# Kernel tuning notes

Measured on AMD Instinct MI355X. Metric: run time of the kernel, lower is better.

The kernel has to match this reference:

```python
import jax, jax.numpy as jnp
import numpy as np

B, S, V, E, HL = 64, 30, 5000, 300, 256
TWOH = 2 * HL
KB, MAPD, MEMD, MLP, NCLS = 512, 512, 512, 1024, 32
L, T, NMOD, NOPS = 8, 9, 9, 6
IH, IW, CIN = 15, 10, 512 + 128


def setup_inputs():
    key = jax.random.key(0)
    ks = iter(jax.random.split(key, 64))
    g = lambda shape, s=0.05: jax.random.normal(next(ks), shape, jnp.float32) * s
    inp = {}
    inp['image'] = g((B, CIN, IH, IW), 1.0)
    inp['ques'] = jax.random.randint(next(ks), (B, S), 0, V)
    ql = jnp.sort(jax.random.randint(next(ks), (B,), 1, S + 1))[::-1]
    inp['q_len'] = ql.at[0].set(S)
    inp['embed_W'] = g((V, E))
    for d in ('f', 'b'):
        inp['lstm_Wi_' + d] = g((E, 4 * HL))
        inp['lstm_Wh_' + d] = g((HL, 4 * HL))
        inp['lstm_b_' + d] = jnp.zeros((4 * HL,), jnp.float32)
    inp['W1'] = g((T, TWOH, TWOH))
    inp['b_1'] = jnp.zeros((TWOH,), jnp.float32)
    inp['W2_w'] = g((2 * TWOH, TWOH)); inp['W2_b'] = jnp.zeros((TWOH,), jnp.float32)
    inp['W3'] = g((TWOH,))
    inp['c_0'] = g((TWOH,), 1.0)
    inp['Wmod'] = g((TWOH, NMOD))
    inp['ic1_w'] = g((KB, CIN)); inp['ic1_b'] = g((KB,), 1.0)
    inp['ic2_w'] = g((KB, KB)); inp['ic2_b'] = g((KB,), 1.0)
    inp['i2m_w'] = g((MAPD, KB)); inp['i2m_b'] = g((MAPD,), 1.0)
    inp['t2m_w'] = g((TWOH, MAPD)); inp['t2m_b'] = jnp.zeros((MAPD,), jnp.float32)
    inp['cell3_ow'] = g((4, NOPS), 1.0)
    inp['cell3_cw'] = g((4, MAPD)); inp['cell3_cb'] = jnp.zeros((4,), jnp.float32)
    inp['cell4_ow'] = g((2, NOPS), 1.0)
    inp['cell4_cw'] = g((2, MAPD)); inp['cell4_cb'] = jnp.zeros((2,), jnp.float32)
    inp['ans_ow'] = g((2, NOPS), 1.0)
    inp['ans_W'] = g((2, 2 * MAPD, MEMD)); inp['ans_b'] = jnp.zeros((2, MEMD), jnp.float32)
    inp['out1_w'] = g((TWOH + MEMD, MLP)); inp['out1_b'] = jnp.zeros((MLP,), jnp.float32)
    inp['out2_w'] = g((MLP, NCLS)); inp['out2_b'] = jnp.zeros((NCLS,), jnp.float32)
    return inp


def _conv1x1(x, w, b):
    return jnp.einsum('bchw,oc->bohw', x, w) + b[None, :, None, None]


def _lstm_dir(xW, Wh, mask, reverse):
    # xW: [S,B,4H], mask: [S,B,1] ; torch LSTM gate order i,f,g,o
    Bn, Hn = xW.shape[1], Wh.shape[0]
    def step(carry, inp):
        h, c = carry
        xw, m = inp
        z = xw + h @ Wh
        i, f, gg, o = jnp.split(z, 4, axis=-1)
        cn = jax.nn.sigmoid(f) * c + jax.nn.sigmoid(i) * jnp.tanh(gg)
        hn = jax.nn.sigmoid(o) * jnp.tanh(cn)
        return (jnp.where(m, hn, h), jnp.where(m, cn, c)), jnp.where(m, hn, 0.0)
    init = (jnp.zeros((Bn, Hn), xW.dtype), jnp.zeros((Bn, Hn), xW.dtype))
    (hF, _), outs = jax.lax.scan(step, init, (xW, mask), reverse=reverse)
    return hF, outs


def _mix3(ow, x, a, t):
    # soft op mixing (DARTS-style) for 3-input cells: x [B,D,H,W], a [B,H,W], t [B,D]
    w = jax.nn.softmax(ow)
    a4 = a[:, None]; t4 = t[:, :, None, None]
    ops = (x * t4, x + t4, x * a4, x * t4 * a4, x, a4 * t4)
    return jax.nn.elu(sum(w[k] * ops[k] for k in range(NOPS)))


def _mix4(ow, x, a1, a2, t):
    w = jax.nn.softmax(ow)
    a14 = a1[:, None]; a24 = a2[:, None]; t4 = t[:, :, None, None]
    ops = (x * t4, x + t4, x * a14, x * a24, x * a14 * a24, x * t4 * (a14 + a24))
    return jax.nn.elu(sum(w[k] * ops[k] for k in range(NOPS)))


def _forward(image, ques, q_len, embed_W, lstm_Wi_f, lstm_Wh_f, lstm_b_f, lstm_Wi_b, lstm_Wh_b, lstm_b_b, W1, b_1, W2_w, W2_b, W3, c_0, Wmod, ic1_w, ic1_b, ic2_w, ic2_b, i2m_w, i2m_b, t2m_w, t2m_b, cell3_ow, cell3_cw, cell3_cb, cell4_ow, cell4_cw, cell4_cb, ans_ow, ans_W, ans_b, out1_w, out1_b, out2_w, out2_b):
    # img_conv (1x1 conv -> ELU -> 1x1 conv)
    x = jax.nn.elu(_conv1x1(image, ic1_w, ic1_b))
    x = _conv1x1(x, ic2_w, ic2_b)
    Bn, _, Hh, Ww = x.shape
    Sn = ques.shape[1]
    # bi-LSTM over the (packed, i.e. masked) question
    emb = embed_W[ques]                                   # [B,S,E]
    mask = (jnp.arange(Sn)[None, :] < q_len[:, None])     # [B,S]
    mT = mask.T[:, :, None].astype(x.dtype) > 0           # [S,B,1] bool
    xWf = (emb @ lstm_Wi_f + lstm_b_f).transpose(1, 0, 2)
    xWb = (emb @ lstm_Wi_b + lstm_b_b).transpose(1, 0, 2)
    hF, oF = _lstm_dir(xWf, lstm_Wh_f, mT, False)
    hB, oB = _lstm_dir(xWb, lstm_Wh_b, mT, True)
    lstm_out = jnp.concatenate([oF, oB], -1).transpose(1, 0, 2)  # [B,S,2H], zero at pads
    q = jnp.concatenate([hF, hB], -1)                            # [B,2H]
    img_map = _conv1x1(x, i2m_w, i2m_b)                          # [B,MAP,H,W]
    stack = jnp.zeros((Bn, Hh, Ww, L), x.dtype)
    p = jnp.zeros((Bn, L), x.dtype).at[:, 0].set(1.0)
    mem = jnp.zeros((Bn, MEMD), x.dtype)
    c_prev = jnp.tile(c_0[None], (Bn, 1))
    e0 = jnp.zeros((L,), x.dtype).at[0].set(1.0)
    imp_loss = jnp.float32(0.0)
    read = lambda st, pp: jnp.einsum('bhwl,bl->bhw', st, pp)
    dec = lambda pp: jnp.concatenate([pp[:, 1:], jnp.zeros_like(pp[:, :1])], 1) + pp * e0
    for t in range(T):
        u = jnp.concatenate([q @ W1[t] + b_1, c_prev], 1) @ W2_w + W2_b  # [B,2H]
        wl = u @ Wmod                                                     # [B,9]
        ls = jax.nn.log_softmax(wl, axis=1)
        imp_loss = imp_loss - jnp.sum(jnp.exp(ls) * ls)
        w = jnp.exp(ls)
        attn = jax.nn.softmax(jnp.einsum('bsh,h->bs', lstm_out * u[:, None, :], W3), axis=1)
        c = jnp.einsum('bs,bsh->bh', attn, lstm_out)
        c_prev = c
        tmap = c @ t2m_w + t2m_b
        stacks, ps = [], []
        a_top = read(stack, p)     # attention at stack top
        # modules 0-3: overwrite at current pointer (pointer shift is commented out in source)
        for m in range(4):
            out = jnp.einsum('bdhw,d->bhw', _mix3(cell3_ow[m], img_map, a_top, tmap), cell3_cw[m]) + cell3_cb[m]
            pb = p[:, None, None, :]
            stacks.append(stack * (1.0 - pb) + out[..., None] * pb)
            ps.append(p)
        # modules 4-5: pop one (soft pointer decrement), then write
        p_dec = dec(p)
        a2 = read(stack, p_dec)
        for m in range(2):
            out = jnp.einsum('bdhw,d->bhw', _mix4(cell4_ow[m], img_map, a_top, a2, tmap), cell4_cw[m]) + cell4_cb[m]
            pb = p_dec[:, None, None, :]
            stacks.append(stack * (1.0 - pb) + out[..., None] * pb)
            ps.append(p_dec)
        # modules 6-7: answer cells -> memory update, stack untouched
        pooled6 = jnp.mean(_mix3(ans_ow[0], img_map, a_top, tmap), axis=(2, 3))
        mem6 = jnp.concatenate([pooled6, tmap], 1) @ ans_W[0] + ans_b[0]
        stacks.append(stack); ps.append(p)
        pooled7 = jnp.mean(_mix4(ans_ow[1], img_map, a_top, a2, tmap), axis=(2, 3))
        mem7 = jnp.concatenate([pooled7, tmap], 1) @ ans_W[1] + ans_b[1]
        stacks.append(stack); ps.append(p_dec)
        # module 8: NoOp
        stacks.append(stack); ps.append(p)
        # soft mixing over modules (the scatter-heavy part)
        stack = jnp.einsum('bm,bmhwl->bhwl', w, jnp.stack(stacks, 1))
        p = jnp.einsum('bm,bml->bl', w, jnp.stack(ps, 1))
        mem = w[:, 6:7] * mem6 + w[:, 7:8] * mem7 + (1.0 - w[:, 6:7] - w[:, 7:8]) * mem
    h1 = jax.nn.elu(jnp.concatenate([q, mem], 1) @ out1_w + out1_b)
    logits = h1 @ out2_w + out2_b
    return logits, imp_loss


def reference(image, ques, q_len, embed_W, lstm_Wi_f, lstm_Wh_f, lstm_b_f, lstm_Wi_b, lstm_Wh_b, lstm_b_b, W1, b_1, W2_w, W2_b, W3, c_0, Wmod, ic1_w, ic1_b, ic2_w, ic2_b, i2m_w, i2m_b, t2m_w, t2m_b, cell3_ow, cell3_cw, cell3_cb, cell4_ow, cell4_cw, cell4_cb, ans_ow, ans_W, ans_b, out1_w, out1_b, out2_w, out2_b):
    return _forward(image, ques, q_len, embed_W, lstm_Wi_f, lstm_Wh_f, lstm_b_f, lstm_Wi_b, lstm_Wh_b, lstm_b_b, W1, b_1, W2_w, W2_b, W3, c_0, Wmod, ic1_w, ic1_b, ic2_w, ic2_b, i2m_w, i2m_b, t2m_w, t2m_b, cell3_ow, cell3_cw, cell3_cb, cell4_ow, cell4_cw, cell4_cb, ans_ow, ans_W, ans_b, out1_w, out1_b, out2_w, out2_b)
```

## Files before the change

kernel.cpp:

```cpp
#include <hip/hip_runtime.h>
#include <hip/hip_fp16.h>
#include <math.h>

#define DEV __device__ __forceinline__

DEV float fexp(float x){ return __expf(x); }
DEV float elu_(float x){ return x > 0.f ? x : fexp(x) - 1.f; }
DEV float sigm_(float x){ return 1.f/(1.f + fexp(-x)); }
DEV float tanh_(float x){ float e = fexp(2.f*x); return 1.f - 2.f/(e + 1.f); }
DEV unsigned bf16r(float x){ unsigned u = __float_as_uint(x);
  return (u + 0x7fffu + ((u>>16)&1u)) >> 16; }
DEV float blo(unsigned u){ return __uint_as_float(u << 16); }
DEV float bhi(unsigned u){ return __uint_as_float(u & 0xffff0000u); }
DEV float bl(unsigned short u){ return __uint_as_float(((unsigned)u) << 16); }

using frag  = __attribute__((ext_vector_type(8))) short;
using fragh = __attribute__((ext_vector_type(8))) _Float16;
using f32x4 = __attribute__((ext_vector_type(4))) float;

DEV uint4 cload16w(const void* p){
  uint4 r;
  asm volatile("global_load_dwordx4 %0, %1, off sc0 sc1\n\ts_waitcnt vmcnt(0)"
               : "=v"(r) : "v"(p) : "memory");
  return r;
}
DEV uint4 cload16nw(const void* p){
  uint4 r;
  asm volatile("global_load_dwordx4 %0, %1, off sc0 sc1"
               : "=v"(r) : "v"(p) : "memory");
  return r;
}

DEV void d_packB(const float* __restrict__ W, short* __restrict__ Bp,
                 int KC, int Ng, int Ksrc, int N, int trans, int idx)
{
  if (idx >= KC*Ng*64) return;
  int lane = idx & 63;
  int g    = (idx >> 6) % Ng;
  int kc   = idx / (64*Ng);
  int n = g*16 + (lane & 15);
  int kb = kc*32 + ((lane >> 4) << 3);
  unsigned o[4];
#pragma unroll
  for (int jj = 0; jj < 4; ++jj) {
    int k0 = kb + 2*jj;
    float v0 = (k0   < Ksrc) ? (trans ? W[(size_t)n*Ksrc + k0]   : W[(size_t)(k0)*N + n])   : 0.f;
    float v1 = (k0+1 < Ksrc) ? (trans ? W[(size_t)n*Ksrc + k0+1] : W[(size_t)(k0+1)*N + n]) : 0.f;
    o[jj] = bf16r(v0) | (bf16r(v1) << 16);
  }
  *(uint4*)(Bp + (size_t)idx*8) = make_uint4(o[0], o[1], o[2], o[3]);
}

DEV void d_packImg(const float* __restrict__ image, short* __restrict__ Ap, int idx)
{
  int lane = idx & 63;
  int kc   = (idx >> 6) % 20;
  int mt   = idx / 1280;
  int row = mt*16 + (lane & 15);
  int b = row / 150, p = row % 150;
  int cb = kc*32 + ((lane >> 4) << 3);
  unsigned o[4];
#pragma unroll
  for (int jj = 0; jj < 4; ++jj) {
    float v0 = image[((size_t)b*640 + cb + 2*jj    )*150 + p];
    float v1 = image[((size_t)b*640 + cb + 2*jj + 1)*150 + p];
    o[jj] = bf16r(v0) | (bf16r(v1) << 16);
  }
  *(uint4*)(Ap + (size_t)idx*8) = make_uint4(o[0], o[1], o[2], o[3]);
}

DEV void d_packEmb(const float* __restrict__ embedW, const int* __restrict__ ques,
                   short* __restrict__ Ap, int idx)
{
  int lane = idx & 63;
  int kc   = (idx >> 6) % 10;
  int mt   = idx / 640;
  int row = mt*16 + (lane & 15);
  int q = ques[row];
  int kb = kc*32 + ((lane >> 4) << 3);
  unsigned o[4];
#pragma unroll
  for (int jj = 0; jj < 4; ++jj) {
    int k0 = kb + 2*jj;
    float v0 = (k0   < 300) ? embedW[(size_t)q*300 + k0]   : 0.f;
    float v1 = (k0+1 < 300) ? embedW[(size_t)q*300 + k0+1] : 0.f;
    o[jj] = bf16r(v0) | (bf16r(v1) << 16);
  }
  *(uint4*)(Ap + (size_t)idx*8) = make_uint4(o[0], o[1], o[2], o[3]);
}

__global__ __launch_bounds__(256)
void megapack_k(const float* __restrict__ c0, const float* __restrict__ c3ow,
                const float* __restrict__ c4ow, const float* __restrict__ aow,
                float* __restrict__ stack, float* __restrict__ pvecA,
                float* __restrict__ mem, float* __restrict__ cprev,
                float* __restrict__ swb, float* __restrict__ pl,
                const float* __restrict__ Whf, const float* __restrict__ Whb,
                unsigned* __restrict__ whT,
                float* __restrict__ hbufz, int* __restrict__ flagz,
                const float* __restrict__ ic1w, short* __restrict__ w1p,
                const float* __restrict__ ic2w, short* __restrict__ w2mp,
                const float* __restrict__ i2mw, short* __restrict__ w3mp,
                const float* __restrict__ Wif, short* __restrict__ wifp,
                const float* __restrict__ Wib, short* __restrict__ wibp,
                const float* __restrict__ image, short* __restrict__ imgP,
                const float* __restrict__ embedW, const int* __restrict__ ques,
                short* __restrict__ embp,
                const float* __restrict__ t2mw, unsigned* __restrict__ t2pp,
                const float* __restrict__ W2w, unsigned short* __restrict__ w2bp,
                const float* __restrict__ ansW, unsigned short* __restrict__ answp)
{
  const int bx = blockIdx.x, tid = threadIdx.x;
  if (bx < 320) {
    int idx = bx*256 + tid;
    int stride = 320*256;
    for (int i = idx; i < 64*150*8; i += stride) stack[i] = 0.f;
    for (int i = idx; i < 64*8;    i += stride) pvecA[i] = ((i & 7) == 0) ? 1.f : 0.f;
    for (int i = idx; i < 64*512;  i += stride) mem[i] = 0.f;
    for (int i = idx; i < 64*512;  i += stride) cprev[i] = c0[i & 511];
    for (int i = idx; i < 9*2*64*512; i += stride) pl[i] = 0.f;
    for (int i = idx; i < 32768;   i += stride) hbufz[i] = 0.f;
    if (idx < 256) flagz[idx] = 0;
    if (idx < 8) {
      const float* ow = (idx < 4) ? (c3ow + idx*6)
                      : (idx < 6) ? (c4ow + (idx-4)*6)
                                  : (aow  + (idx-6)*6);
      float mx = ow[0];
      for (int m = 1; m < 6; ++m) mx = fmaxf(mx, ow[m]);
      float e[6]; float s = 0.f;
      for (int m = 0; m < 6; ++m) { e[m] = fexp(ow[m]-mx); s += e[m]; }
      for (int m = 0; m < 6; ++m) swb[idx*6+m] = e[m]/s;
    }
  } else if (bx < 1344) {
    int idx = (bx-320)*256 + tid;
    int dd  = idx >> 17;
    int rem = idx & 131071;
    int kp  = rem >> 10;
    int zc  = rem & 1023;
    const float* Wh = dd ? Whb : Whf;
    __half2 hv = __floats2half2_rn(Wh[(size_t)(2*kp)*1024 + zc],
                                   Wh[(size_t)(2*kp+1)*1024 + zc]);
    whT[((size_t)dd << 17) + (zc << 7) + kp] = *(unsigned*)&hv;
  } else if (bx < 1504) {
    d_packB(ic1w, w1p, 20, 32, 640, 512, 1, (bx-1344)*256 + tid);
  } else if (bx < 1632) {
    d_packB(ic2w, w2mp, 16, 32, 512, 512, 1, (bx-1504)*256 + tid);
  } else if (bx < 1760) {
    d_packB(i2mw, w3mp, 16, 32, 512, 512, 1, (bx-1632)*256 + tid);
  } else if (bx < 1920) {
    d_packB(Wif, wifp, 10, 64, 300, 1024, 0, (bx-1760)*256 + tid);
  } else if (bx < 2080) {
    d_packB(Wib, wibp, 10, 64, 300, 1024, 0, (bx-1920)*256 + tid);
  } else if (bx < 5080) {
    d_packImg(image, imgP, (bx-2080)*256 + tid);
  } else if (bx < 5380) {
    d_packEmb(embedW, ques, embp, (bx-5080)*256 + tid);
  } else if (bx < 5892) {
    int idx = (bx-5380)*256 + tid;
    int k = idx >> 8, c = idx & 255;
    t2pp[idx] = bf16r(t2mw[(size_t)k*512 + c]) | (bf16r(t2mw[(size_t)k*512 + 256 + c]) << 16);
  } else if (bx < 7940) {
    int i = (bx-5892)*256 + tid;
    w2bp[i] = (unsigned short)bf16r(W2w[i]);
  } else {
    int i = (bx-7940)*256 + tid;
    answp[i] = (unsigned short)bf16r(ansW[i]);
  }
}

__global__ __launch_bounds__(256)
void gemmM_k(const short* __restrict__ ApA, const short* __restrict__ ApB,
             const short* __restrict__ BpA, const short* __restrict__ BpB,
             const float* __restrict__ biasA, const float* __restrict__ biasB,
             void* __restrict__ CoutA, void* __restrict__ CoutB,
             int KC, int Ng, int N, int mode, int act, int KCout)
{
  __shared__ float lds[4][16][68];
  const int z = blockIdx.z;
  const short* Ap = z ? ApB : ApA;
  const short* Bp = z ? BpB : BpA;
  const float* bias = z ? biasB : biasA;
  void* Cout = z ? CoutB : CoutA;
  const int tid = threadIdx.x, lane = tid & 63, w = tid >> 6;
  const int mt = blockIdx.y*4 + w;
  const int ncol0 = blockIdx.x*64;
  const short* Abase = Ap + (((size_t)mt*KC) << 9) + lane*8;
  const short* Bbase = Bp + (((size_t)blockIdx.x*4) << 9) + lane*8;
  f32x4 acc0 = {0.f,0.f,0.f,0.f}, acc1 = acc0, acc2 = acc0, acc3 = acc0;
#pragma unroll 2
  for (int kc = 0; kc < KC; ++kc) {
    frag a = *(const frag*)(Abase + ((size_t)kc << 9));
    const short* bk = Bbase + (((size_t)kc*Ng) << 9);
    frag b0 = *(const frag*)(bk);
    frag b1 = *(const frag*)(bk + 512);
    frag b2 = *(const frag*)(bk + 1024);
    frag b3 = *(const frag*)(bk + 1536);
    acc0 = __builtin_amdgcn_mfma_f32_16x16x32_bf16(a, b0, acc0, 0, 0, 0);
    acc1 = __builtin_amdgcn_mfma_f32_16x16x32_bf16(a, b1, acc1, 0, 0, 0);
    acc2 = __builtin_amdgcn_mfma_f32_16x16x32_bf16(a, b2, acc2, 0, 0, 0);
    acc3 = __builtin_amdgcn_mfma_f32_16x16x32_bf16(a, b3, acc3, 0, 0, 0);
  }
  {
    int colb = lane & 15, rowb = (lane >> 4)*4;
#pragma unroll
    for (int r = 0; r < 4; ++r) {
      lds[w][rowb+r][ 0+colb] = acc0[r];
      lds[w][rowb+r][16+colb] = acc1[r];
      lds[w][rowb+r][32+colb] = acc2[r];
      lds[w][rowb+r][48+colb] = acc3[r];
    }
  }
  __syncthreads();
  if (mode == 0) {
    float* C = (float*)Cout;
    int mloc = lane >> 2, q4 = lane & 3;
    size_t rowoff = (size_t)(mt*16 + mloc)*N + ncol0 + q4*16;
#pragma unroll
    for (int i = 0; i < 4; ++i) {
      float4 v = *(float4*)&lds[w][mloc][q4*16 + i*4];
      const float* bp = bias + ncol0 + q4*16 + i*4;
      v.x += bp[0]; v.y += bp[1]; v.z += bp[2]; v.w += bp[3];
      if (act) { v.x = elu_(v.x); v.y = elu_(v.y); v.z = elu_(v.z); v.w = elu_(v.w); }
      *(float4*)&C[rowoff + i*4] = v;
    }
  } else if (mode == 1) {
    short* C = (short*)Cout;
    int m = lane & 15, qb = (lane >> 4)*8;
#pragma unroll
    for (int h = 0; h < 2; ++h) {
      int nl = h*32 + qb;
      unsigned o[4];
#pragma unroll
      for (int jj = 0; jj < 4; ++jj) {
        float v0 = lds[w][m][nl + 2*jj]     + bias[ncol0 + nl + 2*jj];
        float v1 = lds[w][m][nl + 2*jj + 1] + bias[ncol0 + nl + 2*jj + 1];
        if (act) { v0 = elu_(v0); v1 = elu_(v1); }
        o[jj] = bf16r(v0) | (bf16r(v1) << 16);
      }
      *(uint4*)(C + (((size_t)mt*KCout + (ncol0 >> 5) + h) << 9) + lane*8)
          = make_uint4(o[0], o[1], o[2], o[3]);
    }
  } else {
    unsigned short* C = (unsigned short*)Cout;
    int row = lane >> 2, cb = (lane & 3)*16;
#pragma unroll
    for (int h = 0; h < 2; ++h) {
      unsigned o[4];
#pragma unroll
      for (int jj = 0; jj < 4; ++jj) {
        float v0 = lds[w][row][cb + h*8 + 2*jj]     + bias[ncol0 + cb + h*8 + 2*jj];
        float v1 = lds[w][row][cb + h*8 + 2*jj + 1] + bias[ncol0 + cb + h*8 + 2*jj + 1];
        if (act) { v0 = elu_(v0); v1 = elu_(v1); }
        o[jj] = bf16r(v0) | (bf16r(v1) << 16);
      }
      *(uint4*)&C[(size_t)(mt*16 + row)*N + ncol0 + cb + h*8]
          = make_uint4(o[0], o[1], o[2], o[3]);
    }
  }
}

__global__ __launch_bounds__(512)
void gemm64b_k(const float* __restrict__ A1, long zA1, int K1log,
               const float* __restrict__ A2, int K2,
               const float* __restrict__ B, long zB,
               const float* __restrict__ bias, int zbias,
               float* __restrict__ C, long zC, int N, int act)
{
  const int K1 = 1 << K1log;
  const int Kt = K1 + K2;
  __shared__ __align__(16) float As[8][1024];
  __shared__ float part[8][8][64];
  const int tid = threadIdx.x;
  const int z = blockIdx.z;
  const int r0 = blockIdx.y*8;
  {
    const float* a1 = A1 + (size_t)z*zA1;
    const int nf4 = (8*K1) >> 2;
    for (int e4 = tid; e4 < nf4; e4 += 512) {
      int r = e4 >> (K1log-2);
      int k4 = (e4 & ((K1>>2)-1)) << 2;
      *(float4*)&As[r][k4] = *(const float4*)&a1[(size_t)(r0+r)*K1 + k4];
    }
    if (K2 > 0) {
      for (int e4 = tid; e4 < 1024; e4 += 512) {
        int r = e4 >> 7;
        int k4 = (e4 & 127) << 2;
        *(float4*)&As[r][K1+k4] = *(const float4*)&A2[(size_t)(r0+r)*512 + k4];
      }
    }
  }
  __syncthreads();
  const int lane = tid & 63, w = tid >> 6;
  const int n = blockIdx.x*64 + lane;
  const bool nv = n < N;
  const int kseg = Kt >> 3;
  const int k0 = w*kseg;
  const float* Bp = B + (size_t)z*zB + (size_t)k0*N + (nv ? n : 0);
  float acc[8] = {0,0,0,0,0,0,0,0};
#pragma unroll 8
  for (int kk = 0; kk < kseg; ++kk) {
    float bv = nv ? Bp[(size_t)kk*N] : 0.f;
    int k = k0 + kk;
#pragma unroll
    for (int r = 0; r < 8; ++r) acc[r] += As[r][k]*bv;
  }
#pragma unroll
  for (int r = 0; r < 8; ++r) part[w][r][lane] = acc[r];
  __syncthreads();
  {
    int r = tid >> 6, c = tid & 63;
    int nn = blockIdx.x*64 + c;
    if (nn < N) {
      float s = 0.f;
#pragma unroll
      for (int w2 = 0; w2 < 8; ++w2) s += part[w2][r][c];
      s += bias ? bias[(size_t)z*zbias + nn] : 0.f;
      if (act == 1) s = elu_(s);
      C[(size_t)z*zC + (size_t)(r0+r)*N + nn] = s;
    }
  }
}

__global__ __launch_bounds__(256)
void lstmM_k(const float* __restrict__ xWf, const float* __restrict__ xWb,
             const unsigned* __restrict__ whT, const int* __restrict__ qlen,
             unsigned long long* __restrict__ hbuf, int* __restrict__ flags,
             float* __restrict__ lstm_out, float* __restrict__ qout)
{
  const int bx = blockIdx.x;
  const int d = bx & 1, g = (bx >> 1) & 3, n = bx >> 3;
  const int tid = threadIdx.x, lane = tid & 63, w = tid >> 6;
  const int q = lane >> 4, cl = lane & 15;
  __shared__ __align__(16) unsigned short Wl[65536];

#pragma unroll 4
  for (int rb = 0; rb < 32; ++rb) {
    int lcrow = rb*8 + (tid >> 5);
    int gt = lcrow >> 6, c = lcrow & 63;
    int zc = gt*256 + n*64 + c;
    uint4 v = *(const uint4*)(whT + (((size_t)d*1024 + zc) << 7) + ((tid & 31) << 2));
    int byteoff = (lcrow << 9) + ((((tid & 31) << 4)) ^ ((lcrow & 7) << 4));
    *(uint4*)((char*)Wl + byteoff) = v;
  }

  const float* xW = d ? xWb : xWf;
  const int b   = g*16 + cl;
  const int c4  = w*16 + q*4;
  const int hc4 = n*64 + c4;
  const int len = qlen[b];
  float cst[4] = {0.f,0.f,0.f,0.f}, hst[4] = {0.f,0.f,0.f,0.f};
  int* flg = flags + ((d*4 + g) << 2);
  const int bofs = (cl & 7) << 4;
  __syncthreads();

  for (int ss = 0; ss < 30; ++ss) {
    const int s = d ? (29 - ss) : ss;
    const float* xr = xW + (size_t)b*30720 + (size_t)s*1024 + hc4;
    f32x4 xwv[4];
#pragma unroll
    for (int gt = 0; gt < 4; ++gt) xwv[gt] = *(const f32x4*)(xr + gt*256);

    if (ss > 0) {
      for (;;) {
        uint4 f4 = cload16w(flg);
        if ((int)f4.x >= ss && (int)f4.y >= ss &&
            (int)f4.z >= ss && (int)f4.w >= ss) break;
      }
      __builtin_amdgcn_sched_barrier(0);
    }
    const char* hbr = (const char*)(hbuf + ((size_t)(((ss & 1)*2 + d)*4 + g) << 9))
                    + (cl << 9) + (q << 4);
    union { uint4 u; fragh f; } hv[8];
#pragma unroll
    for (int ks = 0; ks < 8; ++ks) hv[ks].u = cload16nw(hbr + (ks << 6));
    asm volatile("s_waitcnt vmcnt(0)" ::: "memory");
    __builtin_amdgcn_sched_barrier(0);

    f32x4 acc0 = {0.f,0.f,0.f,0.f}, acc1 = acc0, acc2 = acc0, acc3 = acc0;
#pragma unroll
    for (int ks = 0; ks < 8; ++ks) {
      const int kb = ((ks << 6) + (q << 4)) ^ bofs;
      const char* wb = (const char*)Wl + ((w*16 + cl) << 9) + kb;
      fragh a0 = *(const fragh*)(wb);
      fragh a1 = *(const fragh*)(wb + (64 << 9));
      fragh a2 = *(const fragh*)(wb + (128 << 9));
      fragh a3 = *(const fragh*)(wb + (192 << 9));
      acc0 = __builtin_amdgcn_mfma_f32_16x16x32_f16(a0, hv[ks].f, acc0, 0, 0, 0);
      acc1 = __builtin_amdgcn_mfma_f32_16x16x32_f16(a1, hv[ks].f, acc1, 0, 0, 0);
      acc2 = __builtin_amdgcn_mfma_f32_16x16x32_f16(a2, hv[ks].f, acc2, 0, 0, 0);
      acc3 = __builtin_amdgcn_mfma_f32_16x16x32_f16(a3, hv[ks].f, acc3, 0, 0, 0);
    }
    const bool m = s < len;
    f32x4 lo4;
    float hvv[4];
#pragma unroll
    for (int r = 0; r < 4; ++r) {
      float iv = acc0[r] + xwv[0][r];
      float fv = acc1[r] + xwv[1][r];
      float gv = acc2[r] + xwv[2][r];
      float o_ = acc3[r] + xwv[3][r];
      float cn = sigm_(fv)*cst[r] + sigm_(iv)*tanh_(gv);
      float hn = sigm_(o_)*tanh_(cn);
      float hk = m ? hn : hst[r];
      cst[r] = m ? cn : cst[r];
      hst[r] = hk;
      hvv[r] = hk;
      lo4[r] = m ? hn : 0.f;
    }
    unsigned long long* hbw = hbuf + ((size_t)((((ss & 1) ^ 1)*2 + d)*4 + g) << 9);
    union { unsigned long long u; __half2 h2[2]; } hp;
    hp.h2[0] = __floats2half2_rn(hvv[0], hvv[1]);
    hp.h2[1] = __floats2half2_rn(hvv[2], hvv[3]);
    __hip_atomic_store(hbw + cl*64 + (hc4 >> 2), hp.u,
                       __ATOMIC_RELAXED, __HIP_MEMORY_SCOPE_AGENT);
    *(f32x4*)(lstm_out + (((size_t)b*30 + s) << 9) + (d << 8) + hc4) = lo4;
    asm volatile("s_waitcnt vmcnt(0)" ::: "memory");
    __syncthreads();
    if (tid == 0)
      __hip_atomic_store(&flg[n], ss + 1, __ATOMIC_RELAXED, __HIP_MEMORY_SCOPE_AGENT);
  }
  *(f32x4*)(qout + ((size_t)b << 9) + (d << 8) + hc4) =
      f32x4{hst[0], hst[1], hst[2], hst[3]};
}

__global__ __launch_bounds__(1024)
void kcattn3_k(const float* __restrict__ u, const float* __restrict__ Wmod,
               const float* __restrict__ lstm_out, const float* __restrict__ W3,
               const unsigned* __restrict__ t2pp, const float* __restrict__ t2mb,
               float* __restrict__ woutAll, float* __restrict__ imp_part,
               float* __restrict__ cout, float* __restrict__ tmapv, int t)
{
  int b = blockIdx.x;
  int tid = threadIdx.x;
  int lane = tid & 63, wave = tid >> 6;
  __shared__ float ush[512];
  __shared__ float sC[512];
  __shared__ float cpart[512];
  __shared__ float tpart[4][512];
  __shared__ float wl[9];
  __shared__ float sc[32], at[32];
  if (tid < 512) ush[tid] = u[b*512 + tid];
  __syncthreads();
  for (int s = wave; s < 30; s += 16) {
    float acc = 0.f;
    const float* lo = lstm_out + ((size_t)b*30 + s)*512;
#pragma unroll
    for (int h = lane; h < 512; h += 64) acc += lo[h]*ush[h]*W3[h];
#pragma unroll
    for (int off = 32; off; off >>= 1) acc += __shfl_down(acc, off);
    if (lane == 0) sc[s] = acc;
  }
  if (wave < 9) {
    float acc = 0.f;
#pragma unroll
    for (int k = lane; k < 512; k += 64) acc += ush[k]*Wmod[k*9+wave];
#pragma unroll
    for (int off = 32; off; off >>= 1) acc += __shfl_down(acc, off);
    if (lane == 0) wl[wave] = acc;
  }
  __syncthreads();
  if (tid == 0) {
    float mx = wl[0];
    for (int m = 1; m < 9; ++m) mx = fmaxf(mx, wl[m]);
    float s = 0.f;
    for (int m = 0; m < 9; ++m) s += fexp(wl[m]-mx);
    float ls = logf(s);
    float ent = 0.f;
    for (int m = 0; m < 9; ++m) {
      float l = wl[m]-mx-ls;
      float w = fexp(l);
      woutAll[t*576 + b*9 + m] = w;
      ent -= w*l;
    }
    imp_part[t*64+b] = ent;
  }
  if (wave == 1) {
    float v = (lane < 30) ? sc[lane] : -3.4e38f;
    float mx = v;
#pragma unroll
    for (int off = 32; off; off >>= 1) mx = fmaxf(mx, __shfl_xor(mx, off));
    float e = (lane < 30) ? fexp(v-mx) : 0.f;
    float ssum = e;
#pragma unroll
    for (int off = 32; off; off >>= 1) ssum += __shfl_xor(ssum, off);
    if (lane < 30) at[lane] = e/ssum;
  }
  __syncthreads();
  {
    int h = tid & 511, seg = tid >> 9;
    float acc = 0.f;
    int s0 = seg ? 15 : 0, s1 = seg ? 30 : 15;
    for (int s = s0; s < s1; ++s) acc += at[s]*lstm_out[((size_t)b*30 + s)*512 + h];
    if (seg) cpart[h] = acc;
    __syncthreads();
    if (!seg) {
      float tot = acc + cpart[h];
      cout[b*512+h] = tot;
      sC[h] = tot;
    }
  }
  __syncthreads();
  {
    int c2 = tid & 255, ks = tid >> 8;
    float a0 = 0.f, a1 = 0.f;
    const unsigned* tp = t2pp + c2;
#pragma unroll 8
    for (int k = ks*128; k < ks*128 + 128; ++k) {
      float cv = sC[k];
      unsigned wv2 = tp[(size_t)k*256];
      a0 += cv*blo(wv2);
      a1 += cv*bhi(wv2);
    }
    tpart[ks][c2]       = a0;
    tpart[ks][256 + c2] = a1;
  }
  __syncthreads();
  if (tid < 512) {
    float v = tpart[0][tid] + tpart[1][tid] + tpart[2][tid] + tpart[3][tid];
    tmapv[b*512 + tid] = v + t2mb[tid];
  }
}

__global__ __launch_bounds__(256)
void modules2_k(const unsigned short* __restrict__ imapB, const float* __restrict__ tmapv,
                float* __restrict__ stack, const float* __restrict__ pvecIn,
                float* __restrict__ pvecOut,
                const float* __restrict__ swb, const float* __restrict__ c3w,
                const float* __restrict__ c3b, const float* __restrict__ c4w,
                const float* __restrict__ c4b, const float* __restrict__ wmod,
                float* __restrict__ plt)
{
  int b  = blockIdx.x;
  int pb = blockIdx.y;
  int lane = threadIdx.x & 63, wave = threadIdx.x >> 6;
  __shared__ float sT[512];
  __shared__ float pv[8], pd[8], wm[9];
  __shared__ float wpart[4][2][512];
  for (int j = threadIdx.x; j < 512; j += 256) sT[j] = tmapv[b*512 + j];
  if (threadIdx.x < 8) pv[threadIdx.x] = pvecIn[b*8+threadIdx.x];
  if (threadIdx.x >= 64 && threadIdx.x < 73) wm[threadIdx.x-64] = wmod[b*9 + threadIdx.x-64];
  __syncthreads();
  if (threadIdx.x < 8) {
    int l = threadIdx.x;
    pd[l] = (l < 7 ? pv[l+1] : 0.f) + (l == 0 ? pv[0] : 0.f);
  }
  __syncthreads();
  if (pb == 0 && threadIdx.x < 8) {
    int l = threadIdx.x;
    float WP = wm[0]+wm[1]+wm[2]+wm[3] + wm[6] + wm[8];
    float WD = wm[4]+wm[5] + wm[7];
    pvecOut[b*8+l] = WP*pv[l] + WD*pd[l];
  }

  float W[8][6];
#pragma unroll
  for (int m = 0; m < 8; ++m)
#pragma unroll
    for (int i = 0; i < 6; ++i) W[m][i] = swb[m*6+i];
  float W03 = wm[0]+wm[1]+wm[2]+wm[3];
  float W45 = wm[4]+wm[5];

  float acc6[8], acc7[8];
#pragma unroll
  for (int i = 0; i < 8; ++i) { acc6[i] = 0.f; acc7[i] = 0.f; }

  for (int pi = 0; pi < 2; ++pi) {
    int p = pb*8 + wave*2 + pi;
    if (p < 150) {
      const float* st = stack + ((size_t)b*150 + p)*8;
      float a = 0.f, av2 = 0.f;
#pragma unroll
      for (int l = 0; l < 8; ++l) { float v = st[l]; a += v*pv[l]; av2 += v*pd[l]; }
      float part[6] = {0,0,0,0,0,0};
#pragma unroll 2
      for (int i = 0; i < 8; ++i) {
        int d = i*64 + lane;
        float x = bl(imapB[((size_t)b*150 + p)*512 + d]);
        float t = sT[d];
#pragma unroll
        for (int m = 0; m < 4; ++m) {
          float c1 = W[m][0]*t + W[m][1] + W[m][4] + (W[m][2] + W[m][3]*t)*a;
          float c0 = W[m][1]*t + W[m][5]*t*a;
          part[m] += elu_(c1*x + c0) * c3w[m*512+d];
        }
#pragma unroll
        for (int m = 0; m < 2; ++m) {
          float c1 = W[4+m][0]*t + W[4+m][1] + W[4+m][2]*a + W[4+m][3]*av2
                   + W[4+m][4]*a*av2 + W[4+m][5]*t*(a+av2);
          part[4+m] += elu_(c1*x + W[4+m][1]*t) * c4w[m*512+d];
        }
        float c16 = W[6][0]*t + W[6][1] + W[6][4] + (W[6][2] + W[6][3]*t)*a;
        float c06 = W[6][1]*t + W[6][5]*t*a;
        acc6[i] += elu_(c16*x + c06);
        float c17 = W[7][0]*t + W[7][1] + W[7][2]*a + W[7][3]*av2
                  + W[7][4]*a*av2 + W[7][5]*t*(a+av2);
        acc7[i] += elu_(c17*x + W[7][1]*t);
      }
#pragma unroll
      for (int m = 0; m < 6; ++m) {
#pragma unroll
        for (int off = 32; off; off >>= 1) part[m] += __shfl_down(part[m], off);
        part[m] = __shfl(part[m], 0);
      }
      float r3  = wm[0]*(part[0]+c3b[0]) + wm[1]*(part[1]+c3b[1])
                + wm[2]*(part[2]+c3b[2]) + wm[3]*(part[3]+c3b[3]);
      float r45 = wm[4]*(part[4]+c4b[0]) + wm[5]*(part[5]+c4b[1]);
      if (lane < 8) {
        int l = lane;
        size_t idx = ((size_t)b*150 + p)*8 + l;
        stack[idx] = stack[idx]*(1.f - W03*pv[l] - W45*pd[l])
                   + pv[l]*r3 + pd[l]*r45;
      }
    }
  }
#pragma unroll
  for (int i = 0; i < 8; ++i) {
    wpart[wave][0][i*64+lane] = acc6[i];
    wpart[wave][1][i*64+lane] = acc7[i];
  }
  __syncthreads();
  for (int e = threadIdx.x; e < 1024; e += 256) {
    int which = e >> 9, d = e & 511;
    float s = wpart[0][which][d] + wpart[1][which][d]
            + wpart[2][which][d] + wpart[3][which][d];
    atomicAdd(&plt[(size_t)which*32768 + b*512 + d], s * (1.f/150.f));
  }
}

__global__ __launch_bounds__(512)
void ansu3_k(const float* __restrict__ plt, const float* __restrict__ tmapv,
             const unsigned short* __restrict__ answp, const float* __restrict__ ansb,
             float* __restrict__ m67o,
             const float* __restrict__ tmp1n, const float* __restrict__ cprev,
             const unsigned short* __restrict__ w2bp, const float* __restrict__ W2b,
             float* __restrict__ ubuf, int do_u)
{
  const int z = blockIdx.z;
  if (z == 2 && !do_u) return;
  __shared__ __align__(16) float As[8][1024];
  __shared__ float part[8][8][64];
  const int tid = threadIdx.x;
  const int r0 = blockIdx.y*8;
  const int nc0 = blockIdx.x*64;
  const int lane = tid & 63, w = tid >> 6;

  if (z < 2) {
    for (int e4 = tid; e4 < 1024; e4 += 512) {
      int r = e4 >> 7, k4 = (e4 & 127) << 2;
      *(float4*)&As[r][k4]     = *(const float4*)&plt[(size_t)z*32768 + (size_t)(r0+r)*512 + k4];
      *(float4*)&As[r][512+k4] = *(const float4*)&tmapv[(size_t)(r0+r)*512 + k4];
    }
  } else {
    for (int e4 = tid; e4 < 1024; e4 += 512) {
      int r = e4 >> 7, k4 = (e4 & 127) << 2;
      *(float4*)&As[r][k4]     = *(const float4*)&tmp1n[(size_t)(r0+r)*512 + k4];
      *(float4*)&As[r][512+k4] = *(const float4*)&cprev[(size_t)(r0+r)*512 + k4];
    }
  }
  __syncthreads();
  {
    const unsigned short* Bp = (z < 2 ? answp + (size_t)z*524288 : w2bp)
                             + (size_t)(w*128)*512 + nc0 + lane;
    float acc[8] = {0,0,0,0,0,0,0,0};
    int k0 = w*128;
#pragma unroll 8
    for (int kk = 0; kk < 128; ++kk) {
      float bv = bl(Bp[(size_t)kk*512]);
#pragma unroll
      for (int r = 0; r < 8; ++r) acc[r] += As[r][k0+kk]*bv;
    }
#pragma unroll
    for (int r = 0; r < 8; ++r) part[w][r][lane] = acc[r];
  }
  __syncthreads();
  {
    int r = tid >> 6, c = tid & 63;
    float s = 0.f;
#pragma unroll
    for (int w2 = 0; w2 < 8; ++w2) s += part[w2][r][c];
    if (z < 2) {
      m67o[((size_t)z*64 + r0 + r)*512 + nc0 + c] = s + ansb[z*512 + nc0 + c];
    } else {
      ubuf[(size_t)(r0+r)*512 + nc0 + c] = s + W2b[nc0 + c];
    }
  }
}

__global__ __launch_bounds__(512)
void memfin_k(const float* __restrict__ woutAll, const float* __restrict__ m67t,
              float* __restrict__ memb)
{
  int b = blockIdx.x;
  int tid = threadIdx.x;
  __shared__ float w6s[9], w7s[9], coef[9];
  if (tid < 9)       w6s[tid] = woutAll[tid*576 + b*9 + 6];
  else if (tid < 18) w7s[tid-9] = woutAll[(tid-9)*576 + b*9 + 7];
  __syncthreads();
  if (tid == 0) {
    float c = 1.f;
    for (int t = 8; t >= 0; --t) { coef[t] = c; c *= (1.f - w6s[t] - w7s[t]); }
  }
  __syncthreads();
  float acc = 0.f;
#pragma unroll
  for (int t = 0; t < 9; ++t) {
    float m6 = m67t[(((size_t)t*2 + 0)*64 + b)*512 + tid];
    float m7 = m67t[(((size_t)t*2 + 1)*64 + b)*512 + tid];
    acc += coef[t]*(w6s[t]*m6 + w7s[t]*m7);
  }
  memb[b*512 + tid] = acc;
}

__global__ __launch_bounds__(256)
void imp_k(const float* __restrict__ part, float* __restrict__ out)
{
  int lane = threadIdx.x & 63, wave = threadIdx.x >> 6;
  float acc = 0.f;
  for (int i = threadIdx.x; i < 576; i += 256) acc += part[i];
#pragma unroll
  for (int off = 32; off; off >>= 1) acc += __shfl_down(acc, off);
  __shared__ float red[4];
  if (lane == 0) red[wave] = acc;
  __syncthreads();
  if (threadIdx.x == 0) out[0] = red[0]+red[1]+red[2]+red[3];
}

extern "C" void kernel_launch(void* const* d_in, const int* in_sizes, int n_in,
                              void* d_out, int out_size, void* d_ws, size_t ws_size,
                              hipStream_t stream)
{
  (void)in_sizes; (void)n_in; (void)out_size; (void)ws_size;
  const float* image = (const float*)d_in[0];
  const int*   ques  = (const int*)d_in[1];
  const int*   qlen  = (const int*)d_in[2];
  const float* embedW= (const float*)d_in[3];
  const float* Wi_f  = (const float*)d_in[4];
  const float* Wh_f  = (const float*)d_in[5];
  const float* b_f   = (const float*)d_in[6];
  const float* Wi_b  = (const float*)d_in[7];
  const float* Wh_b  = (const float*)d_in[8];
  const float* b_b   = (const float*)d_in[9];
  const float* W1    = (const float*)d_in[10];
  const float* b1    = (const float*)d_in[11];
  const float* W2w   = (const float*)d_in[12];
  const float* W2b   = (const float*)d_in[13];
  const float* W3    = (const float*)d_in[14];
  const float* c0    = (const float*)d_in[15];
  const float* Wmod  = (const float*)d_in[16];
  const float* ic1w  = (const float*)d_in[17];
  const float* ic1b  = (const float*)d_in[18];
  const float* ic2w  = (const float*)d_in[19];
  const float* ic2b  = (const float*)d_in[20];
  const float* i2mw  = (const float*)d_in[21];
  const float* i2mb  = (const float*)d_in[22];
  const float* t2mw  = (const float*)d_in[23];
  const float* t2mb  = (const float*)d_in[24];
  const float* c3ow  = (const float*)d_in[25];
  const float* c3cw  = (const float*)d_in[26];
  const float* c3cb  = (const float*)d_in[27];
  const float* c4ow  = (const float*)d_in[28];
  const float* c4cw  = (const float*)d_in[29];
  const float* c4cb  = (const float*)d_in[30];
  const float* aow   = (const float*)d_in[31];
  const float* ansW  = (const float*)d_in[32];
  const float* ansb  = (const float*)d_in[33];
  const float* o1w   = (const float*)d_in[34];
  const float* o1b   = (const float*)d_in[35];
  const float* o2w   = (const float*)d_in[36];
  const float* o2b   = (const float*)d_in[37];
  float* out = (float*)d_out;
  float* ws  = (float*)d_ws;

  size_t off = 0;
  auto alloc = [&](size_t n){ float* p = ws + off; off += n; return p; };
  short* imgP  = (short*)alloc(600ull*20*64*8/2);
  short* X1p   = (short*)alloc(600ull*16*64*8/2);
  short* X2p   = (short*)alloc(600ull*16*64*8/2);
  short* w1p   = (short*)alloc(20*32*64*8/2);
  short* w2mp  = (short*)alloc(16*32*64*8/2);
  short* w3mp  = (short*)alloc(16*32*64*8/2);
  short* wifp  = (short*)alloc(10*64*64*8/2);
  short* wibp  = (short*)alloc(10*64*64*8/2);
  short* embp  = (short*)alloc(120ull*10*64*8/2);
  unsigned short* imapB = (unsigned short*)alloc(9600ull*512/2);
  unsigned* t2pp = (unsigned*)alloc(512*256);
  unsigned short* w2bp  = (unsigned short*)alloc(524288/2);
  unsigned short* answp = (unsigned short*)alloc(1048576/2);
  float* xWfb  = alloc(64ull*30*1024);
  float* xWbb  = alloc(64ull*30*1024);
  float* lout  = alloc(64ull*30*512);
  float* qbuf  = alloc(64*512);
  float* stck  = alloc(64*150*8);
  float* pvecA = alloc(64*8);
  float* pvecB = alloc(64*8);
  float* memb  = alloc(64*512);
  float* cprev = alloc(64*512);
  float* tmp1a = alloc(9ull*64*512);
  float* ubuf  = alloc(64*512);
  float* wmwA  = alloc(9*64*9);
  float* impp  = alloc(9*64);
  float* swb   = alloc(48);
  float* pl    = alloc(9ull*2*64*512);
  float* m67t  = alloc(9ull*2*64*512);
  float* tmapv = alloc(64*512);
  float* h1b   = alloc(64*1024);
  unsigned* whT = (unsigned*)alloc(2ull*1024*128);
  float* hbufW  = alloc(32768);
  int*   flagsI = (int*)alloc(256);

  megapack_k<<<12036, 256, 0, stream>>>(
      c0, c3ow, c4ow, aow, stck, pvecA, memb, cprev, swb, pl,
      Wh_f, Wh_b, whT, hbufW, flagsI,
      ic1w, w1p, ic2w, w2mp, i2mw, w3mp, Wi_f, wifp, Wi_b, wibp,
      image, imgP, embedW, ques, embp, t2mw, t2pp,
      W2w, w2bp, ansW, answp);

  gemmM_k<<<dim3(8,150,1), 256, 0, stream>>>(imgP, imgP, w1p, w1p, ic1b, ic1b,
                                             X1p, X1p, 20, 32, 512, 1, 1, 16);
  gemmM_k<<<dim3(8,150,1), 256, 0, stream>>>(X1p, X1p, w2mp, w2mp, ic2b, ic2b,
                                             X2p, X2p, 16, 32, 512, 1, 0, 16);
  gemmM_k<<<dim3(8,150,1), 256, 0, stream>>>(X2p, X2p, w3mp, w3mp, i2mb, i2mb,
                                             imapB, imapB, 16, 32, 512, 2, 0, 0);
  gemmM_k<<<dim3(16,30,2), 256, 0, stream>>>(embp, embp, wifp, wibp, b_f, b_b,
                                             xWfb, xWbb, 10, 64, 1024, 0, 0, 0);

  lstmM_k<<<32, 256, 0, stream>>>(xWfb, xWbb, whT, qlen,
                                  (unsigned long long*)hbufW, flagsI, lout, qbuf);

  gemm64b_k<<<dim3(8,8,9), 512, 0, stream>>>(
      qbuf, 0, 9, (const float*)nullptr, 0,
      W1, 262144, b1, 0, tmp1a, 32768, 512, 0);
  gemm64b_k<<<dim3(8,8,1), 512, 0, stream>>>(
      tmp1a, 0, 9, cprev, 512, W2w, 0, W2b, 0, ubuf, 0, 512, 0);

  for (int t = 0; t < 9; ++t) {
    float* pvIn  = (t & 1) ? pvecB : pvecA;
    float* pvOut = (t & 1) ? pvecA : pvecB;
    kcattn3_k<<<64, 1024, 0, stream>>>(ubuf, Wmod, lout, W3, t2pp, t2mb,
                                       wmwA, impp, cprev, tmapv, t);
    modules2_k<<<dim3(64,19), 256, 0, stream>>>(
        imapB, tmapv, stck, pvIn, pvOut, swb, c3cw, c3cb, c4cw, c4cb,
        wmwA + (size_t)t*576, pl + (size_t)t*65536);
    ansu3_k<<<dim3(8,8,3), 512, 0, stream>>>(
        pl + (size_t)t*65536, tmapv, answp, ansb, m67t + (size_t)t*65536,
        tmp1a + (size_t)(t < 8 ? t+1 : 0)*32768, cprev, w2bp, W2b, ubuf,
        (t < 8) ? 1 : 0);
  }

  memfin_k<<<64, 512, 0, stream>>>(wmwA, m67t, memb);
  gemm64b_k<<<dim3(16,8,1), 512, 0, stream>>>(
      qbuf, 0, 9, memb, 512, o1w, 0, o1b, 0, h1b, 0, 1024, 1);
  gemm64b_k<<<dim3(1,8,1), 512, 0, stream>>>(
      h1b, 0, 10, (const float*)nullptr, 0, o2w, 0, o2b, 0, out, 0, 32, 0);
  imp_k<<<1, 256, 0, stream>>>(impp, out + 2048);
}
```

Before: 854.9 us.

## Replace LSTM flag handshake with sentinel-filled per-step hidden-state buffers

The cross-block LSTM recurrence used to publish h into a double buffer, then wait on vmcnt, run a block barrier and write a per-block flag that consumers polled before reading h. Now every timestep gets its own hidden-state slot, pre-filled with an all-ones half sentinel (NaN pattern), and consumers poll the h data directly until no sentinel halves remain. This removes the store drain, the barrier and the flag round trip from the serial critical path. In exchange it uses a larger buffer that must be filled every call, and it relies on real fp16 h values never equalling 0xFFFF and on each 16-byte load seeing a consistent snapshot.

```diff
diff --git a/kernel.cpp b/kernel.cpp
--- a/kernel.cpp
+++ b/kernel.cpp
@@ -18,17 +18,15 @@
 using fragh = __attribute__((ext_vector_type(8))) _Float16;
 using f32x4 = __attribute__((ext_vector_type(4))) float;
 
-DEV uint4 cload16w(const void* p){
-  uint4 r;
-  asm volatile("global_load_dwordx4 %0, %1, off sc0 sc1\n\ts_waitcnt vmcnt(0)"
-               : "=v"(r) : "v"(p) : "memory");
-  return r;
-}
 DEV uint4 cload16nw(const void* p){
   uint4 r;
   asm volatile("global_load_dwordx4 %0, %1, off sc0 sc1"
                : "=v"(r) : "v"(p) : "memory");
   return r;
+}
+DEV void cstore8(void* p, unsigned long long v){
+  asm volatile("global_store_dwordx2 %0, %1, off sc0 sc1"
+               :: "v"(p), "v"(v) : "memory");
 }
 
 DEV void d_packB(const float* __restrict__ W, short* __restrict__ Bp,
@@ -97,7 +95,7 @@
                 float* __restrict__ swb, float* __restrict__ pl,
                 const float* __restrict__ Whf, const float* __restrict__ Whb,
                 unsigned* __restrict__ whT,
-                float* __restrict__ hbufz, int* __restrict__ flagz,
+                float* __restrict__ hbufz,
                 const float* __restrict__ ic1w, short* __restrict__ w1p,
                 const float* __restrict__ ic2w, short* __restrict__ w2mp,
                 const float* __restrict__ i2mw, short* __restrict__ w3mp,
@@ -119,8 +117,8 @@
     for (int i = idx; i < 64*512;  i += stride) mem[i] = 0.f;
     for (int i = idx; i < 64*512;  i += stride) cprev[i] = c0[i & 511];
     for (int i = idx; i < 9*2*64*512; i += stride) pl[i] = 0.f;
-    for (int i = idx; i < 32768;   i += stride) hbufz[i] = 0.f;
-    if (idx < 256) flagz[idx] = 0;
+    for (int i = idx; i < 491520; i += stride)
+      hbufz[i] = __uint_as_float(0xFFFFFFFFu);
     if (idx < 8) {
       const float* ow = (idx < 4) ? (c3ow + idx*6)
                       : (idx < 6) ? (c4ow + (idx-4)*6)
@@ -324,7 +322,7 @@
 __global__ __launch_bounds__(256)
 void lstmM_k(const float* __restrict__ xWf, const float* __restrict__ xWb,
              const unsigned* __restrict__ whT, const int* __restrict__ qlen,
-             unsigned long long* __restrict__ hbuf, int* __restrict__ flags,
+             unsigned long long* __restrict__ hbuf,
              float* __restrict__ lstm_out, float* __restrict__ qout)
 {
   const int bx = blockIdx.x;
@@ -349,8 +347,7 @@
   const int hc4 = n*64 + c4;
   const int len = qlen[b];
   float cst[4] = {0.f,0.f,0.f,0.f}, hst[4] = {0.f,0.f,0.f,0.f};
-  int* flg = flags + ((d*4 + g) << 2);
-  const int bofs = (cl & 7) << 4;
+  const int grp = d*4 + g;
   __syncthreads();
 
   for (int ss = 0; ss < 30; ++ss) {
@@ -360,35 +357,41 @@
 #pragma unroll
     for (int gt = 0; gt < 4; ++gt) xwv[gt] = *(const f32x4*)(xr + gt*256);
 
+    f32x4 acc0 = {0.f,0.f,0.f,0.f}, acc1 = acc0, acc2 = acc0, acc3 = acc0;
     if (ss > 0) {
+      const char* hbr = (const char*)(hbuf + ((size_t)((ss-1)*8 + grp) << 10))
+                      + (cl << 9) + (q << 4);
+      union { uint4 u; fragh f; } hv[8];
       for (;;) {
-        uint4 f4 = cload16w(flg);
-        if ((int)f4.x >= ss && (int)f4.y >= ss &&
-            (int)f4.z >= ss && (int)f4.w >= ss) break;
+#pragma unroll
+        for (int ks = 0; ks < 8; ++ks) hv[ks].u = cload16nw(hbr + (ks << 6));
+        asm volatile("s_waitcnt vmcnt(0)" ::: "memory");
+        bool ok = true;
+#pragma unroll
+        for (int ks = 0; ks < 8; ++ks) {
+          unsigned a = hv[ks].u.x, b2 = hv[ks].u.y,
+                   c = hv[ks].u.z, e = hv[ks].u.w;
+          ok &= ((a & 0xFFFFu) != 0xFFFFu) && ((a >> 16) != 0xFFFFu);
+          ok &= ((b2 & 0xFFFFu) != 0xFFFFu) && ((b2 >> 16) != 0xFFFFu);
+          ok &= ((c & 0xFFFFu) != 0xFFFFu) && ((c >> 16) != 0xFFFFu);
+          ok &= ((e & 0xFFFFu) != 0xFFFFu) && ((e >> 16) != 0xFFFFu);
+        }
+        if (ok) break;
       }
       __builtin_amdgcn_sched_barrier(0);
-    }
-    const char* hbr = (const char*)(hbuf + ((size_t)(((ss & 1)*2 + d)*4 + g) << 9))
-                    + (cl << 9) + (q << 4);
-    union { uint4 u; fragh f; } hv[8];
-#pragma unroll
-    for (int ks = 0; ks < 8; ++ks) hv[ks].u = cload16nw(hbr + (ks << 6));
-    asm volatile("s_waitcnt vmcnt(0)" ::: "memory");
-    __builtin_amdgcn_sched_barrier(0);
-
-    f32x4 acc0 = {0.f,0.f,0.f,0.f}, acc1 = acc0, acc2 = acc0, acc3 = acc0;
-#pragma unroll
-    for (int ks = 0; ks < 8; ++ks) {
-      const int kb = ((ks << 6) + (q << 4)) ^ bofs;
-      const char* wb = (const char*)Wl + ((w*16 + cl) << 9) + kb;
-      fragh a0 = *(const fragh*)(wb);
-      fragh a1 = *(const fragh*)(wb + (64 << 9));
-      fragh a2 = *(const fragh*)(wb + (128 << 9));
-      fragh a3 = *(const fragh*)(wb + (192 << 9));
-      acc0 = __builtin_amdgcn_mfma_f32_16x16x32_f16(a0, hv[ks].f, acc0, 0, 0, 0);
-      acc1 = __builtin_amdgcn_mfma_f32_16x16x32_f16(a1, hv[ks].f, acc1, 0, 0, 0);
-      acc2 = __builtin_amdgcn_mfma_f32_16x16x32_f16(a2, hv[ks].f, acc2, 0, 0, 0);
-      acc3 = __builtin_amdgcn_mfma_f32_16x16x32_f16(a3, hv[ks].f, acc3, 0, 0, 0);
+#pragma unroll
+      for (int ks = 0; ks < 8; ++ks) {
+        const int kb = ((ks << 6) + (q << 4)) ^ ((cl & 7) << 4);
+        const char* wb = (const char*)Wl + ((w*16 + cl) << 9) + kb;
+        fragh a0 = *(const fragh*)(wb);
+        fragh a1 = *(const fragh*)(wb + (64 << 9));
+        fragh a2 = *(const fragh*)(wb + (128 << 9));
+        fragh a3 = *(const fragh*)(wb + (192 << 9));
+        acc0 = __builtin_amdgcn_mfma_f32_16x16x32_f16(a0, hv[ks].f, acc0, 0, 0, 0);
+        acc1 = __builtin_amdgcn_mfma_f32_16x16x32_f16(a1, hv[ks].f, acc1, 0, 0, 0);
+        acc2 = __builtin_amdgcn_mfma_f32_16x16x32_f16(a2, hv[ks].f, acc2, 0, 0, 0);
+        acc3 = __builtin_amdgcn_mfma_f32_16x16x32_f16(a3, hv[ks].f, acc3, 0, 0, 0);
+      }
     }
     const bool m = s < len;
     f32x4 lo4;
@@ -407,17 +410,12 @@
       hvv[r] = hk;
       lo4[r] = m ? hn : 0.f;
     }
-    unsigned long long* hbw = hbuf + ((size_t)((((ss & 1) ^ 1)*2 + d)*4 + g) << 9);
+    unsigned long long* hbw = hbuf + ((size_t)(ss*8 + grp) << 10);
     union { unsigned long long u; __half2 h2[2]; } hp;
     hp.h2[0] = __floats2half2_rn(hvv[0], hvv[1]);
     hp.h2[1] = __floats2half2_rn(hvv[2], hvv[3]);
-    __hip_atomic_store(hbw + cl*64 + (hc4 >> 2), hp.u,
-                       __ATOMIC_RELAXED, __HIP_MEMORY_SCOPE_AGENT);
+    cstore8(hbw + cl*64 + (hc4 >> 2), hp.u);
     *(f32x4*)(lstm_out + (((size_t)b*30 + s) << 9) + (d << 8) + hc4) = lo4;
-    asm volatile("s_waitcnt vmcnt(0)" ::: "memory");
-    __syncthreads();
-    if (tid == 0)
-      __hip_atomic_store(&flg[n], ss + 1, __ATOMIC_RELAXED, __HIP_MEMORY_SCOPE_AGENT);
   }
   *(f32x4*)(qout + ((size_t)b << 9) + (d << 8) + hc4) =
       f32x4{hst[0], hst[1], hst[2], hst[3]};
@@ -805,12 +803,11 @@
   float* tmapv = alloc(64*512);
   float* h1b   = alloc(64*1024);
   unsigned* whT = (unsigned*)alloc(2ull*1024*128);
-  float* hbufW  = alloc(32768);
-  int*   flagsI = (int*)alloc(256);
+  float* hbufW  = alloc(491520);
 
   megapack_k<<<12036, 256, 0, stream>>>(
       c0, c3ow, c4ow, aow, stck, pvecA, memb, cprev, swb, pl,
-      Wh_f, Wh_b, whT, hbufW, flagsI,
+      Wh_f, Wh_b, whT, hbufW,
       ic1w, w1p, ic2w, w2mp, i2mw, w3mp, Wi_f, wifp, Wi_b, wibp,
       image, imgP, embedW, ques, embp, t2mw, t2pp,
       W2w, w2bp, ansW, answp);
@@ -825,7 +822,7 @@
                                              xWfb, xWbb, 10, 64, 1024, 0, 0, 0);
 
   lstmM_k<<<32, 256, 0, stream>>>(xWfb, xWbb, whT, qlen,
-                                  (unsigned long long*)hbufW, flagsI, lout, qbuf);
+                                  (unsigned long long*)hbufW, lout, qbuf);
 
   gemm64b_k<<<dim3(8,8,9), 512, 0, stream>>>(
       qbuf, 0, 9, (const float*)nullptr, 0,
```

After: 872.0 us. About the same (+2.0%).

## Fuse W2 control projection into attention kernel and batch answer GEMMs after loop

Applied to the files above, without the earlier changes.

The per-step u = [tmp1,cprev]·W2 projection moves inside kcattn3_k, where each of the 64 blocks computes its own row with 1024 threads. This removes the separate gemm64b launch and the z=2 slice of ansu3. The answer-module GEMMs for all 9 steps are deferred into a single ansall_k launch after the loop, which needs tmapv stored per step. The loop goes from three launches per step to two. The cost is a serial 512-deep dot product per thread inside the attention kernel, which lengthens that kernel.

```diff
diff --git a/kernel.cpp b/kernel.cpp
--- a/kernel.cpp
+++ b/kernel.cpp
@@ -424,7 +424,9 @@
 }
 
 __global__ __launch_bounds__(1024)
-void kcattn3_k(const float* __restrict__ u, const float* __restrict__ Wmod,
+void kcattn3_k(const float* __restrict__ tmp1, const float* __restrict__ cprevB,
+               const unsigned short* __restrict__ w2bp, const float* __restrict__ W2b,
+               const float* __restrict__ Wmod,
                const float* __restrict__ lstm_out, const float* __restrict__ W3,
                const unsigned* __restrict__ t2pp, const float* __restrict__ t2mb,
                float* __restrict__ woutAll, float* __restrict__ imp_part,
@@ -433,13 +435,28 @@
   int b = blockIdx.x;
   int tid = threadIdx.x;
   int lane = tid & 63, wave = tid >> 6;
+  __shared__ float A2s[1024];
   __shared__ float ush[512];
+  __shared__ float upart[512];
   __shared__ float sC[512];
   __shared__ float cpart[512];
   __shared__ float tpart[4][512];
   __shared__ float wl[9];
   __shared__ float sc[32], at[32];
-  if (tid < 512) ush[tid] = u[b*512 + tid];
+  if (tid < 512) A2s[tid] = tmp1[b*512 + tid];
+  else           A2s[tid] = cprevB[b*512 + (tid - 512)];
+  __syncthreads();
+  {
+    int col = tid & 511, kh = tid >> 9;
+    const unsigned short* wp = w2bp + ((size_t)kh*512)*512 + col;
+    const float* av = A2s + kh*512;
+    float acc = 0.f;
+#pragma unroll 8
+    for (int k = 0; k < 512; ++k) acc += av[k]*bl(wp[(size_t)k*512]);
+    if (kh) upart[col] = acc;
+    __syncthreads();
+    if (!kh) ush[col] = acc + upart[col] + W2b[col];
+  }
   __syncthreads();
   for (int s = wave; s < 30; s += 16) {
     float acc = 0.f;
@@ -628,15 +645,12 @@
 }
 
 __global__ __launch_bounds__(512)
-void ansu3_k(const float* __restrict__ plt, const float* __restrict__ tmapv,
-             const unsigned short* __restrict__ answp, const float* __restrict__ ansb,
-             float* __restrict__ m67o,
-             const float* __restrict__ tmp1n, const float* __restrict__ cprev,
-             const unsigned short* __restrict__ w2bp, const float* __restrict__ W2b,
-             float* __restrict__ ubuf, int do_u)
+void ansall_k(const float* __restrict__ plt, const float* __restrict__ tmapv,
+              const unsigned short* __restrict__ answp, const float* __restrict__ ansb,
+              float* __restrict__ m67o)
 {
   const int z = blockIdx.z;
-  if (z == 2 && !do_u) return;
+  const int t = z >> 1, zz = z & 1;
   __shared__ __align__(16) float As[8][1024];
   __shared__ float part[8][8][64];
   const int tid = threadIdx.x;
@@ -644,22 +658,14 @@
   const int nc0 = blockIdx.x*64;
   const int lane = tid & 63, w = tid >> 6;
 
-  if (z < 2) {
-    for (int e4 = tid; e4 < 1024; e4 += 512) {
-      int r = e4 >> 7, k4 = (e4 & 127) << 2;
-      *(float4*)&As[r][k4]     = *(const float4*)&plt[(size_t)z*32768 + (size_t)(r0+r)*512 + k4];
-      *(float4*)&As[r][512+k4] = *(const float4*)&tmapv[(size_t)(r0+r)*512 + k4];
-    }
-  } else {
-    for (int e4 = tid; e4 < 1024; e4 += 512) {
-      int r = e4 >> 7, k4 = (e4 & 127) << 2;
-      *(float4*)&As[r][k4]     = *(const float4*)&tmp1n[(size_t)(r0+r)*512 + k4];
-      *(float4*)&As[r][512+k4] = *(const float4*)&cprev[(size_t)(r0+r)*512 + k4];
-    }
+  for (int e4 = tid; e4 < 1024; e4 += 512) {
+    int r = e4 >> 7, k4 = (e4 & 127) << 2;
+    *(float4*)&As[r][k4]     = *(const float4*)&plt[(size_t)z*32768 + (size_t)(r0+r)*512 + k4];
+    *(float4*)&As[r][512+k4] = *(const float4*)&tmapv[(size_t)t*32768 + (size_t)(r0+r)*512 + k4];
   }
   __syncthreads();
   {
-    const unsigned short* Bp = (z < 2 ? answp + (size_t)z*524288 : w2bp)
+    const unsigned short* Bp = answp + (size_t)zz*524288
                              + (size_t)(w*128)*512 + nc0 + lane;
     float acc[8] = {0,0,0,0,0,0,0,0};
     int k0 = w*128;
@@ -678,11 +684,7 @@
     float s = 0.f;
 #pragma unroll
     for (int w2 = 0; w2 < 8; ++w2) s += part[w2][r][c];
-    if (z < 2) {
-      m67o[((size_t)z*64 + r0 + r)*512 + nc0 + c] = s + ansb[z*512 + nc0 + c];
-    } else {
-      ubuf[(size_t)(r0+r)*512 + nc0 + c] = s + W2b[nc0 + c];
-    }
+    m67o[(size_t)z*32768 + (size_t)(r0+r)*512 + nc0 + c] = s + ansb[zz*512 + nc0 + c];
   }
 }
 
@@ -796,13 +798,12 @@
   float* memb  = alloc(64*512);
   float* cprev = alloc(64*512);
   float* tmp1a = alloc(9ull*64*512);
-  float* ubuf  = alloc(64*512);
   float* wmwA  = alloc(9*64*9);
   float* impp  = alloc(9*64);
   float* swb   = alloc(48);
   float* pl    = alloc(9ull*2*64*512);
   float* m67t  = alloc(9ull*2*64*512);
-  float* tmapv = alloc(64*512);
+  float* tmapv = alloc(9ull*64*512);
   float* h1b   = alloc(64*1024);
   unsigned* whT = (unsigned*)alloc(2ull*1024*128);
   float* hbufW  = alloc(32768);
@@ -830,22 +831,21 @@
   gemm64b_k<<<dim3(8,8,9), 512, 0, stream>>>(
       qbuf, 0, 9, (const float*)nullptr, 0,
       W1, 262144, b1, 0, tmp1a, 32768, 512, 0);
-  gemm64b_k<<<dim3(8,8,1), 512, 0, stream>>>(
-      tmp1a, 0, 9, cprev, 512, W2w, 0, W2b, 0, ubuf, 0, 512, 0);
 
   for (int t = 0; t < 9; ++t) {
     float* pvIn  = (t & 1) ? pvecB : pvecA;
     float* pvOut = (t & 1) ? pvecA : pvecB;
-    kcattn3_k<<<64, 1024, 0, stream>>>(ubuf, Wmod, lout, W3, t2pp, t2mb,
-                                       wmwA, impp, cprev, tmapv, t);
+    kcattn3_k<<<64, 1024, 0, stream>>>(
+        tmp1a + (size_t)t*32768, cprev, w2bp, W2b,
+        Wmod, lout, W3, t2pp, t2mb,
+        wmwA, impp, cprev, tmapv + (size_t)t*32768, t);
     modules2_k<<<dim3(64,19), 256, 0, stream>>>(
-        imapB, tmapv, stck, pvIn, pvOut, swb, c3cw, c3cb, c4cw, c4cb,
+        imapB, tmapv + (size_t)t*32768, stck, pvIn, pvOut, swb,
+        c3cw, c3cb, c4cw, c4cb,
         wmwA + (size_t)t*576, pl + (size_t)t*65536);
-    ansu3_k<<<dim3(8,8,3), 512, 0, stream>>>(
-        pl + (size_t)t*65536, tmapv, answp, ansb, m67t + (size_t)t*65536,
-        tmp1a + (size_t)(t < 8 ? t+1 : 0)*32768, cprev, w2bp, W2b, ubuf,
-        (t < 8) ? 1 : 0);
-  }
+  }
+
+  ansall_k<<<dim3(8,8,18), 512, 0, stream>>>(pl, tmapv, answp, ansb, m67t);
 
   memfin_k<<<64, 512, 0, stream>>>(wmwA, m67t, memb);
   gemm64b_k<<<dim3(16,8,1), 512, 0, stream>>>(
```

New measurement: 947.7 us. +10.9%, slower.
